# Kernel tuning notes

Measured on AMD Instinct MI355X. Metric: run time of the kernel, lower is better.

The kernel has to match this reference:

```python
import jax, jax.numpy as jnp
import numpy as np

N = 100000   # nodes
D = 8        # in_dim/2 (per-node phase dim)
H = 256      # hidden_dim
E = 1600000  # directed edges (avg degree 16)


def setup_inputs() -> dict:
    key = jax.random.key(0)
    ks = jax.random.split(key, 8)
    q = jax.random.normal(ks[0], (N, D), jnp.float32)
    p = jax.random.normal(ks[1], (N, D), jnp.float32)
    # per-node diagonal positive-definite mass matrix (what get_mass() produces:
    # diag(relu(diag(.)) + 1e-4)); keep it well-conditioned for the inverse.
    m_diag = jax.random.uniform(ks[2], (N, D), jnp.float32) + 0.5
    M = jax.vmap(jnp.diag)(m_diag)  # [N, D, D]
    src = jax.random.randint(ks[3], (E,), 0, N, dtype=jnp.int32)
    off = jax.random.randint(ks[4], (E,), 1, N, dtype=jnp.int32)
    dst = ((src + off) % N).astype(jnp.int32)  # guaranteed no self-edges (euclid>0)
    W1 = jax.random.normal(ks[5], (D, H), jnp.float32) / jnp.sqrt(D)
    b1 = jnp.zeros((H,), jnp.float32)
    W2 = jax.random.normal(ks[6], (H, D), jnp.float32) / jnp.sqrt(H)
    b2 = jnp.zeros((D,), jnp.float32)
    gravity = jnp.ones((1, 1), jnp.float32)
    return {"q": q, "p": p, "M": M, "src": src, "dst": dst,
            "W1": W1, "b1": b1, "W2": W2, "b2": b2, "gravity": gravity}


def _gcn(x, src, dst, norm_src, norm_dst, W, b, n_nodes):
    # DGL GraphConv norm='both': D_out^{-1/2} on src, sum-aggregate, D_in^{-1/2} on dst
    m = (x * norm_src[:, None])[src]                       # [E, F]
    agg = jax.ops.segment_sum(m, dst, num_segments=n_nodes)
    return (agg * norm_dst[:, None]) @ W + b


def reference(q, p, M, src, dst, W1, b1, W2, b2, gravity):
    n = q.shape[0]
    ones_e = jnp.ones(src.shape[0], q.dtype)
    out_deg = jax.ops.segment_sum(ones_e, src, num_segments=n)
    in_deg = jax.ops.segment_sum(ones_e, dst, num_segments=n)
    norm_src = jnp.where(out_deg > 0, out_deg, 1.0) ** -0.5
    norm_dst = jnp.where(in_deg > 0, in_deg, 1.0) ** -0.5

    def P_scalar(qq):
        # ConvGNN: GraphConv -> ReLU -> GraphConv, residual add
        h = jax.nn.relu(_gcn(qq, src, dst, norm_src, norm_dst, W1, b1, n))
        h = _gcn(h, src, dst, norm_src, norm_dst, W2, b2, n) + qq      # [N, D]
        euclid = jnp.linalg.norm(h[src] - h[dst], axis=-1)             # [E]
        masses = M[src] * M[dst]                                       # [E, D, D]
        return 0.5 * jnp.sum(gravity[0, 0] * masses / euclid[:, None, None])

    # dHdq = grad of potential P w.r.t q (torch.autograd.grad in original)
    dHdQ = jax.grad(P_scalar)(q)
    # dHdp: per-node p_i @ inv(M_i)  (self-loop graph, degree 1 per node)
    dHdP = jnp.linalg.solve(jnp.swapaxes(M, -1, -2), p[..., None])[..., 0]
    return jnp.concatenate([dHdQ, dHdP], axis=-1)  # [N, 2D]
```

## Files before the change

### kernel.cpp

```cpp
#include <hip/hip_runtime.h>
#include <hip/hip_fp16.h>

#define DD 8
#define HH 256
#define CH 8192
#define PAYBITS 17
#define PAYMASK 0x1FFFF
#define WPITCH 20


__global__ void k_coarse(const int* __restrict__ src, const int* __restrict__ dst,
                         int* __restrict__ gHistIn, int* __restrict__ gHistOut,
                         int NB, int E) {
    __shared__ int hIn[256], hOut[256];
    if (threadIdx.x < 256) { hIn[threadIdx.x] = 0; hOut[threadIdx.x] = 0; }
    __syncthreads();
    int lo = blockIdx.x * CH;
    int hi = min(lo + CH, E);
    for (int i = lo + threadIdx.x; i < hi; i += blockDim.x) {
        atomicAdd(&hIn[dst[i] >> 9], 1);
        atomicAdd(&hOut[src[i] >> 9], 1);
    }
    __syncthreads();
    if (threadIdx.x < NB) {
        int ci = hIn[threadIdx.x], co = hOut[threadIdx.x];
        if (ci) atomicAdd(&gHistIn[threadIdx.x], ci);
        if (co) atomicAdd(&gHistOut[threadIdx.x], co);
    }
}

__global__ void k_cscan(const int* __restrict__ gHistIn, const int* __restrict__ gHistOut,
                        int* __restrict__ cStartIn, int* __restrict__ cStartOut,
                        int* __restrict__ cCurIn, int* __restrict__ cCurOut,
                        int NB, int E) {
    __shared__ int s[256];
#pragma unroll
    for (int dir = 0; dir < 2; dir++) {
        const int* gh = dir ? gHistOut : gHistIn;
        int* cs = dir ? cStartOut : cStartIn;
        int* cc = dir ? cCurOut : cCurIn;
        int v = (threadIdx.x < NB) ? gh[threadIdx.x] : 0;
        s[threadIdx.x] = v;
        __syncthreads();
        for (int off = 1; off < 256; off <<= 1) {
            int t = (threadIdx.x >= off) ? s[threadIdx.x - off] : 0;
            __syncthreads();
            s[threadIdx.x] += t;
            __syncthreads();
        }
        if (threadIdx.x < NB) {
            int ex = s[threadIdx.x] - v;
            cs[threadIdx.x] = ex;
            cc[threadIdx.x] = ex;
        }
        if (threadIdx.x == 0) cs[NB] = E;
        __syncthreads();
    }
}

__global__ void k_part2(const int* __restrict__ src, const int* __restrict__ dst,
                        int* __restrict__ cCurIn, int* __restrict__ cCurOut,
                        int* __restrict__ P_in, int* __restrict__ P_out,
                        int NB, int E) {
    int dir = blockIdx.y;
    const int* key = dir ? src : dst;
    const int* pay = dir ? dst : src;
    int* cCur = dir ? cCurOut : cCurIn;
    int* P    = dir ? P_out   : P_in;
    __shared__ int h[256];
    if (threadIdx.x < 256) h[threadIdx.x] = 0;
    __syncthreads();
    int lo = blockIdx.x * CH;
    int hi = min(lo + CH, E);
    for (int i = lo + threadIdx.x; i < hi; i += blockDim.x)
        atomicAdd(&h[key[i] >> 9], 1);
    __syncthreads();
    if (threadIdx.x < NB) {
        int c = h[threadIdx.x];
        h[threadIdx.x] = c ? atomicAdd(&cCur[threadIdx.x], c) : 0;
    }
    __syncthreads();
    for (int i = lo + threadIdx.x; i < hi; i += blockDim.x) {
        int k = key[i];
        int pos = atomicAdd(&h[k >> 9], 1);
        P[pos] = ((k & 511) << PAYBITS) | pay[i];
    }
}

__launch_bounds__(512)
__global__ void k_fine2(const int* __restrict__ cStartIn, const int* __restrict__ cStartOut,
                        const int* __restrict__ P_in, const int* __restrict__ P_out,
                        int* __restrict__ start_in, int* __restrict__ start_out,
                        int* __restrict__ csr_in, int* __restrict__ csr_out, int N) {
    int dir = blockIdx.y;
    const int* cStart = dir ? cStartOut : cStartIn;
    const int* P      = dir ? P_out     : P_in;
    int* start        = dir ? start_out : start_in;
    int* csr          = dir ? csr_out   : csr_in;
    __shared__ int cnt[512], scn[512];
    int b = blockIdx.x;
    int lo = cStart[b], hi = cStart[b + 1];
    cnt[threadIdx.x] = 0;
    __syncthreads();
    for (int i = lo + threadIdx.x; i < hi; i += 512)
        atomicAdd(&cnt[P[i] >> PAYBITS], 1);
    __syncthreads();
    int own = cnt[threadIdx.x];
    scn[threadIdx.x] = own;
    __syncthreads();
    for (int off = 1; off < 512; off <<= 1) {
        int t = (threadIdx.x >= off) ? scn[threadIdx.x - off] : 0;
        __syncthreads();
        scn[threadIdx.x] += t;
        __syncthreads();
    }
    int base = lo + scn[threadIdx.x] - own;
    int node = (b << 9) + threadIdx.x;
    if (node < N) start[node] = base;
    cnt[threadIdx.x] = base;
    __syncthreads();
    for (int i = lo + threadIdx.x; i < hi; i += 512) {
        int p = P[i];
        int pos = atomicAdd(&cnt[p >> PAYBITS], 1);
        csr[pos] = p & PAYMASK;
    }
}

__global__ void k_prep(const float* __restrict__ q, const float* __restrict__ p,
                       const float* __restrict__ M,
                       const float* __restrict__ W1, const float* __restrict__ W2,
                       float* __restrict__ W12p,
                       int* __restrict__ start_in, int* __restrict__ start_out,
                       float* __restrict__ a, float* __restrict__ b,
                       __half2* __restrict__ hm, float* __restrict__ qn,
                       float* __restrict__ out, int N, int E) {
    int t = blockIdx.x * blockDim.x + threadIdx.x;
    if (t == 0) { start_in[N] = E; start_out[N] = E; }
    if (t < HH * DD) {
        int j = t >> 3, dd = t & 7;
        W12p[j * WPITCH + dd]     = W1[dd * HH + j];
        W12p[j * WPITCH + 8 + dd] = W2[j * DD + dd];
    }
    int v = t;
    if (v >= N) return;
    int ei1 = (v + 1 < N) ? start_in[v + 1]  : E;
    int eo1 = (v + 1 < N) ? start_out[v + 1] : E;
    float din  = (float)(ei1 - start_in[v]);
    float dout = (float)(eo1 - start_out[v]);
    float av = 1.0f / sqrtf(dout > 0.f ? dout : 1.f);
    float bv = 1.0f / sqrtf(din  > 0.f ? din  : 1.f);
    a[v] = av; b[v] = bv;
#pragma unroll
    for (int d = 0; d < DD; d++) {
        float m = M[(size_t)v * DD * DD + d * (DD + 1)];
        __half2 hmv;
        hmv.x = __float2half(0.f);
        hmv.y = __float2half(m);
        hm[(size_t)v * DD + d] = hmv;
        qn[(size_t)v * DD + d] = av * q[(size_t)v * DD + d];
        out[(size_t)v * 2 * DD + DD + d] = p[(size_t)v * DD + d] / m;
    }
}

static __device__ __forceinline__
void acc_h8(uint4 r, float acc[8]) {
    float2 f;
    f = __half22float2(*(__half2*)&r.x); acc[0] += f.x; acc[1] += f.y;
    f = __half22float2(*(__half2*)&r.y); acc[2] += f.x; acc[3] += f.y;
    f = __half22float2(*(__half2*)&r.z); acc[4] += f.x; acc[5] += f.y;
    f = __half22float2(*(__half2*)&r.w); acc[6] += f.x; acc[7] += f.y;
}

static __device__ __forceinline__
void unpack_hm(uint4 r0, uint4 r1, float h[8], float m[8]) {
    float2 f;
    f = __half22float2(*(__half2*)&r0.x); h[0] = f.x; m[0] = f.y;
    f = __half22float2(*(__half2*)&r0.y); h[1] = f.x; m[1] = f.y;
    f = __half22float2(*(__half2*)&r0.z); h[2] = f.x; m[2] = f.y;
    f = __half22float2(*(__half2*)&r0.w); h[3] = f.x; m[3] = f.y;
    f = __half22float2(*(__half2*)&r1.x); h[4] = f.x; m[4] = f.y;
    f = __half22float2(*(__half2*)&r1.y); h[5] = f.x; m[5] = f.y;
    f = __half22float2(*(__half2*)&r1.z); h[6] = f.x; m[6] = f.y;
    f = __half22float2(*(__half2*)&r1.w); h[7] = f.x; m[7] = f.y;
}

static __device__ __forceinline__
void gather_h8(const int* __restrict__ csr, const __half* __restrict__ x,
               int e, int e1, float acc[8]) {
    for (; e + 3 < e1; e += 4) {
        int u0 = csr[e], u1 = csr[e + 1], u2 = csr[e + 2], u3 = csr[e + 3];
        uint4 r0 = *(const uint4*)(x + (size_t)u0 * DD);
        uint4 r1 = *(const uint4*)(x + (size_t)u1 * DD);
        uint4 r2 = *(const uint4*)(x + (size_t)u2 * DD);
        uint4 r3 = *(const uint4*)(x + (size_t)u3 * DD);
        acc_h8(r0, acc); acc_h8(r1, acc); acc_h8(r2, acc); acc_h8(r3, acc);
    }
    for (; e < e1; e++) {
        uint4 r = *(const uint4*)(x + (size_t)csr[e] * DD);
        acc_h8(r, acc);
    }
}


__launch_bounds__(256)
__global__ void k_agg_node(const int* __restrict__ start, const int* __restrict__ csr,
                           const float* __restrict__ x, float* __restrict__ y, int N) {
    int t = blockIdx.x * 256 + threadIdx.x;
    int v = t >> 1, half = t & 1;
    if (v >= N) return;
    int e0 = start[v], e1 = start[v + 1];
    int mid = e0 + ((e1 - e0) >> 1);
    int e = half ? mid : e0, hi = half ? e1 : mid;
    float acc[8] = {0.f, 0.f, 0.f, 0.f, 0.f, 0.f, 0.f, 0.f};
    for (; e + 1 < hi; e += 2) {
        int u0 = csr[e], u1 = csr[e + 1];
        const float4* p0 = (const float4*)(x + (size_t)u0 * DD);
        const float4* p1 = (const float4*)(x + (size_t)u1 * DD);
        float4 a0 = p0[0], b0 = p0[1], a1 = p1[0], b1 = p1[1];
        acc[0] += a0.x + a1.x; acc[1] += a0.y + a1.y;
        acc[2] += a0.z + a1.z; acc[3] += a0.w + a1.w;
        acc[4] += b0.x + b1.x; acc[5] += b0.y + b1.y;
        acc[6] += b0.z + b1.z; acc[7] += b0.w + b1.w;
    }
    if (e < hi) {
        const float4* p = (const float4*)(x + (size_t)csr[e] * DD);
        float4 a0 = p[0], b0 = p[1];
        acc[0] += a0.x; acc[1] += a0.y; acc[2] += a0.z; acc[3] += a0.w;
        acc[4] += b0.x; acc[5] += b0.y; acc[6] += b0.z; acc[7] += b0.w;
    }
#pragma unroll
    for (int k = 0; k < 8; k++) acc[k] += __shfl_xor(acc[k], 1);
    if (!half) {
        float4* yp = (float4*)(y + (size_t)v * DD);
        yp[0] = make_float4(acc[0], acc[1], acc[2], acc[3]);
        yp[1] = make_float4(acc[4], acc[5], acc[6], acc[7]);
    }
}

__launch_bounds__(256)
__global__ void k_h_node(const int* __restrict__ start, const int* __restrict__ csr,
                         const __half* __restrict__ ya, const float* __restrict__ b,
                         const float* __restrict__ q, const float* __restrict__ b2,
                         __half2* __restrict__ hm, int N) {
    int t = blockIdx.x * 256 + threadIdx.x;
    int v = t >> 1, half = t & 1;
    if (v >= N) return;
    int e0 = start[v], e1 = start[v + 1];
    int mid = e0 + ((e1 - e0) >> 1);
    float acc[8] = {0.f, 0.f, 0.f, 0.f, 0.f, 0.f, 0.f, 0.f};
    gather_h8(csr, ya, half ? mid : e0, half ? e1 : mid, acc);
#pragma unroll
    for (int k = 0; k < 8; k++) acc[k] += __shfl_xor(acc[k], 1);
    if (!half) {
        float bv = b[v];
        const float4* qp = (const float4*)(q + (size_t)v * DD);
        float4 q0 = qp[0], q1 = qp[1];
        float hq[8] = {q0.x, q0.y, q0.z, q0.w, q1.x, q1.y, q1.z, q1.w};
        __half2* hp = hm + (size_t)v * DD;
#pragma unroll
        for (int k = 0; k < DD; k++) {
            float hval = fmaf(bv, acc[k], b2[k] + hq[k]);
            __half2 cur = hp[k];
            cur.x = __float2half(hval);
            hp[k] = cur;
        }
    }
}

__launch_bounds__(256)
__global__ void k_gh4(const int* __restrict__ start_in, const int* __restrict__ csr_in,
                      const int* __restrict__ start_out, const int* __restrict__ csr_out,
                      const __half2* __restrict__ hm,
                      const float* __restrict__ b, const float* __restrict__ grav,
                      float* __restrict__ gh, __half* __restrict__ bgh, int N) {
    int t = blockIdx.x * 256 + threadIdx.x;
    int v = t >> 2, sub = t & 3, dir = sub >> 1, half = sub & 1;
    if (v >= N) return;
    const uint4* srec = (const uint4*)(hm + (size_t)v * DD);
    uint4 s0 = srec[0], s1 = srec[1];
    float hv[8], mv[8];
    unpack_hm(s0, s1, hv, mv);
    const int* start = dir ? start_out : start_in;
    const int* csr   = dir ? csr_out   : csr_in;
    int e0 = start[v], e1 = start[v + 1];
    int mid = e0 + ((e1 - e0) >> 1);
    int e = half ? mid : e0, hi = half ? e1 : mid;
    float coef = -0.5f * grav[0];
    float acc[8] = {0.f, 0.f, 0.f, 0.f, 0.f, 0.f, 0.f, 0.f};
    for (; e + 1 < hi; e += 2) {
        int u0 = csr[e], u1 = csr[e + 1];
        const uint4* r0p = (const uint4*)(hm + (size_t)u0 * DD);
        const uint4* r1p = (const uint4*)(hm + (size_t)u1 * DD);
        uint4 x0 = r0p[0], x1 = r0p[1], y0 = r1p[0], y1 = r1p[1];
        float hu0[8], mu0[8], hu1[8], mu1[8];
        unpack_hm(x0, x1, hu0, mu0);
        unpack_hm(y0, y1, hu1, mu1);
        float d0[8], d1[8];
        float e20 = 0.f, S0 = 0.f, e21 = 0.f, S1 = 0.f;
#pragma unroll
        for (int k = 0; k < 8; k++) {
            d0[k] = hv[k] - hu0[k];
            d1[k] = hv[k] - hu1[k];
            e20 = fmaf(d0[k], d0[k], e20);
            e21 = fmaf(d1[k], d1[k], e21);
            S0 = fmaf(mv[k], mu0[k], S0);
            S1 = fmaf(mv[k], mu1[k], S1);
        }
        float r0 = rsqrtf(e20), r1 = rsqrtf(e21);
        float c0 = coef * S0 * r0 * r0 * r0;
        float c1 = coef * S1 * r1 * r1 * r1;
#pragma unroll
        for (int k = 0; k < 8; k++)
            acc[k] = fmaf(c0, d0[k], fmaf(c1, d1[k], acc[k]));
    }
    if (e < hi) {
        int u = csr[e];
        const uint4* rp = (const uint4*)(hm + (size_t)u * DD);
        uint4 x0 = rp[0], x1 = rp[1];
        float hu[8], mu[8];
        unpack_hm(x0, x1, hu, mu);
        float df[8];
        float e2 = 0.f, S = 0.f;
#pragma unroll
        for (int k = 0; k < 8; k++) {
            df[k] = hv[k] - hu[k];
            e2 = fmaf(df[k], df[k], e2);
            S = fmaf(mv[k], mu[k], S);
        }
        float r = rsqrtf(e2);
        float c = coef * S * r * r * r;
#pragma unroll
        for (int k = 0; k < 8; k++) acc[k] = fmaf(c, df[k], acc[k]);
    }
#pragma unroll
    for (int k = 0; k < 8; k++) acc[k] += __shfl_xor(acc[k], 1);
#pragma unroll
    for (int k = 0; k < 8; k++) acc[k] += __shfl_xor(acc[k], 2);
    if (sub == 0) {
        float4* gp = (float4*)(gh + (size_t)v * DD);
        gp[0] = make_float4(acc[0], acc[1], acc[2], acc[3]);
        gp[1] = make_float4(acc[4], acc[5], acc[6], acc[7]);
        float bv = b[v];
        __half2* bp = (__half2*)(bgh + (size_t)v * DD);
        bp[0] = __floats2half2_rn(bv * acc[0], bv * acc[1]);
        bp[1] = __floats2half2_rn(bv * acc[2], bv * acc[3]);
        bp[2] = __floats2half2_rn(bv * acc[4], bv * acc[5]);
        bp[3] = __floats2half2_rn(bv * acc[6], bv * acc[7]);
    }
}

__launch_bounds__(256)
__global__ void k_bgh_node(const int* __restrict__ start, const int* __restrict__ csr,
                           const __half* __restrict__ bgh, float* __restrict__ gq2, int N) {
    int t = blockIdx.x * 256 + threadIdx.x;
    int v = t >> 1, half = t & 1;
    if (v >= N) return;
    int e0 = start[v], e1 = start[v + 1];
    int mid = e0 + ((e1 - e0) >> 1);
    float acc[8] = {0.f, 0.f, 0.f, 0.f, 0.f, 0.f, 0.f, 0.f};
    gather_h8(csr, bgh, half ? mid : e0, half ? e1 : mid, acc);
#pragma unroll
    for (int k = 0; k < 8; k++) acc[k] += __shfl_xor(acc[k], 1);
    if (!half) {
        float4* yp = (float4*)(gq2 + (size_t)v * DD);
        yp[0] = make_float4(acc[0], acc[1], acc[2], acc[3]);
        yp[1] = make_float4(acc[4], acc[5], acc[6], acc[7]);
    }
}

__launch_bounds__(256)
__global__ void k_out_node(const int* __restrict__ start, const int* __restrict__ csr,
                           const __half* __restrict__ gz1b, const float* __restrict__ gh,
                           const float* __restrict__ a, float* __restrict__ out, int N) {
    int t = blockIdx.x * 256 + threadIdx.x;
    int v = t >> 1, half = t & 1;
    if (v >= N) return;
    int e0 = start[v], e1 = start[v + 1];
    int mid = e0 + ((e1 - e0) >> 1);
    float acc[8] = {0.f, 0.f, 0.f, 0.f, 0.f, 0.f, 0.f, 0.f};
    gather_h8(csr, gz1b, half ? mid : e0, half ? e1 : mid, acc);
#pragma unroll
    for (int k = 0; k < 8; k++) acc[k] += __shfl_xor(acc[k], 1);
    if (!half) {
        float av = a[v];
        const float4* gp = (const float4*)(gh + (size_t)v * DD);
        float4 g0 = gp[0], g1 = gp[1];
        float4* op = (float4*)(out + (size_t)v * 2 * DD);
        op[0] = make_float4(fmaf(av, acc[0], g0.x), fmaf(av, acc[1], g0.y),
                            fmaf(av, acc[2], g0.z), fmaf(av, acc[3], g0.w));
        op[1] = make_float4(fmaf(av, acc[4], g1.x), fmaf(av, acc[5], g1.y),
                            fmaf(av, acc[6], g1.z), fmaf(av, acc[7], g1.w));
    }
}


__launch_bounds__(256)
__global__ void k_mlp_fwd(const float* __restrict__ agg1, const float* __restrict__ a,
                          const float* __restrict__ b,
                          const float* __restrict__ W12p, const float* __restrict__ b1,
                          __half* __restrict__ ya, int N) {
    __shared__ float sW[HH * WPITCH];
    __shared__ float sb1[HH];
    for (int i = threadIdx.x; i < HH * WPITCH; i += 256) sW[i] = W12p[i];
    for (int i = threadIdx.x; i < HH; i += 256) sb1[i] = b1[i];
    __syncthreads();
    int t = blockIdx.x * 256 + threadIdx.x;
    int v = t >> 4, l16 = t & 15, sub = (t >> 3) & 1, d = t & 7;
    if (v >= N) return;
    float zl = b[v] * agg1[(size_t)v * DD + d];
    float z[DD];
#pragma unroll
    for (int k = 0; k < DD; k++) z[k] = __shfl(zl, k, 16);
    float acc[DD] = {0.f, 0.f, 0.f, 0.f, 0.f, 0.f, 0.f, 0.f};
    for (int c = 0; c < HH / 16; c += 2) {
        int j0 = (c << 4) | l16, j1 = j0 + 16;
        const float4* w0 = (const float4*)(sW + j0 * WPITCH);
        const float4* w1 = (const float4*)(sW + j1 * WPITCH);
        float4 wa0 = w0[0], wb0 = w0[1], va0 = w0[2], vb0 = w0[3];
        float4 wa1 = w1[0], wb1 = w1[1], va1 = w1[2], vb1 = w1[3];
        float ua0 = fmaf(z[1], wa0.y, fmaf(z[0], wa0.x, sb1[j0]));
        ua0 = fmaf(z[3], wa0.w, fmaf(z[2], wa0.z, ua0));
        float ub0 = fmaf(z[5], wb0.y, z[4] * wb0.x);
        ub0 = fmaf(z[7], wb0.w, fmaf(z[6], wb0.z, ub0));
        float ua1 = fmaf(z[1], wa1.y, fmaf(z[0], wa1.x, sb1[j1]));
        ua1 = fmaf(z[3], wa1.w, fmaf(z[2], wa1.z, ua1));
        float ub1 = fmaf(z[5], wb1.y, z[4] * wb1.x);
        ub1 = fmaf(z[7], wb1.w, fmaf(z[6], wb1.z, ub1));
        float h0 = fmaxf(ua0 + ub0, 0.f);
        float h1 = fmaxf(ua1 + ub1, 0.f);
        acc[0] = fmaf(h0, va0.x, acc[0]); acc[1] = fmaf(h0, va0.y, acc[1]);
        acc[2] = fmaf(h0, va0.z, acc[2]); acc[3] = fmaf(h0, va0.w, acc[3]);
        acc[4] = fmaf(h0, vb0.x, acc[4]); acc[5] = fmaf(h0, vb0.y, acc[5]);
        acc[6] = fmaf(h0, vb0.z, acc[6]); acc[7] = fmaf(h0, vb0.w, acc[7]);
        acc[0] = fmaf(h1, va1.x, acc[0]); acc[1] = fmaf(h1, va1.y, acc[1]);
        acc[2] = fmaf(h1, va1.z, acc[2]); acc[3] = fmaf(h1, va1.w, acc[3]);
        acc[4] = fmaf(h1, vb1.x, acc[4]); acc[5] = fmaf(h1, vb1.y, acc[5]);
        acc[6] = fmaf(h1, vb1.z, acc[6]); acc[7] = fmaf(h1, vb1.w, acc[7]);
    }
#pragma unroll
    for (int m = 1; m < 16; m <<= 1)
#pragma unroll
        for (int k = 0; k < DD; k++) acc[k] += __shfl_xor(acc[k], m);
    float yl = acc[0];
#pragma unroll
    for (int k = 1; k < DD; k++) yl = (d == k) ? acc[k] : yl;
    if (!sub) ya[(size_t)v * DD + d] = __float2half(a[v] * yl);
}

__launch_bounds__(256)
__global__ void k_mlp_bwd(const float* __restrict__ gq2, const float* __restrict__ agg1,
                          const float* __restrict__ a, const float* __restrict__ b,
                          const float* __restrict__ W12p, const float* __restrict__ b1,
                          __half* __restrict__ gz1b, int N) {
    __shared__ float sW[HH * WPITCH];
    __shared__ float sb1[HH];
    for (int i = threadIdx.x; i < HH * WPITCH; i += 256) sW[i] = W12p[i];
    for (int i = threadIdx.x; i < HH; i += 256) sb1[i] = b1[i];
    __syncthreads();
    int t = blockIdx.x * 256 + threadIdx.x;
    int v = t >> 4, l16 = t & 15, sub = (t >> 3) & 1, d = t & 7;
    if (v >= N) return;
    float bv = b[v], av = a[v];
    float zl = bv * agg1[(size_t)v * DD + d];
    float gl = gq2[(size_t)v * DD + d];
    float z[DD], gq[DD];
#pragma unroll
    for (int k = 0; k < DD; k++) { z[k] = __shfl(zl, k, 16); gq[k] = __shfl(gl, k, 16); }
    float gz[DD] = {0.f, 0.f, 0.f, 0.f, 0.f, 0.f, 0.f, 0.f};
    for (int c = 0; c < HH / 16; c += 2) {
        int j0 = (c << 4) | l16, j1 = j0 + 16;
        const float4* w0 = (const float4*)(sW + j0 * WPITCH);
        const float4* w1 = (const float4*)(sW + j1 * WPITCH);
        float4 wa0 = w0[0], wb0 = w0[1], va0 = w0[2], vb0 = w0[3];
        float4 wa1 = w1[0], wb1 = w1[1], va1 = w1[2], vb1 = w1[3];
        float ua0 = fmaf(z[1], wa0.y, fmaf(z[0], wa0.x, sb1[j0]));
        ua0 = fmaf(z[3], wa0.w, fmaf(z[2], wa0.z, ua0));
        float ub0 = fmaf(z[5], wb0.y, z[4] * wb0.x);
        ub0 = fmaf(z[7], wb0.w, fmaf(z[6], wb0.z, ub0));
        float ua1 = fmaf(z[1], wa1.y, fmaf(z[0], wa1.x, sb1[j1]));
        ua1 = fmaf(z[3], wa1.w, fmaf(z[2], wa1.z, ua1));
        float ub1 = fmaf(z[5], wb1.y, z[4] * wb1.x);
        ub1 = fmaf(z[7], wb1.w, fmaf(z[6], wb1.z, ub1));
        float u0 = ua0 + ub0, u1 = ua1 + ub1;
        float ga0 = fmaf(gq[1], va0.y, gq[0] * va0.x);
        ga0 = fmaf(gq[3], va0.w, fmaf(gq[2], va0.z, ga0));
        float gb0 = fmaf(gq[5], vb0.y, gq[4] * vb0.x);
        gb0 = fmaf(gq[7], vb0.w, fmaf(gq[6], vb0.z, gb0));
        float ga1 = fmaf(gq[1], va1.y, gq[0] * va1.x);
        ga1 = fmaf(gq[3], va1.w, fmaf(gq[2], va1.z, ga1));
        float gb1 = fmaf(gq[5], vb1.y, gq[4] * vb1.x);
        gb1 = fmaf(gq[7], vb1.w, fmaf(gq[6], vb1.z, gb1));
        float g0 = (u0 > 0.f) ? av * (ga0 + gb0) : 0.f;
        float g1 = (u1 > 0.f) ? av * (ga1 + gb1) : 0.f;
        gz[0] = fmaf(g0, wa0.x, gz[0]); gz[1] = fmaf(g0, wa0.y, gz[1]);
        gz[2] = fmaf(g0, wa0.z, gz[2]); gz[3] = fmaf(g0, wa0.w, gz[3]);
        gz[4] = fmaf(g0, wb0.x, gz[4]); gz[5] = fmaf(g0, wb0.y, gz[5]);
        gz[6] = fmaf(g0, wb0.z, gz[6]); gz[7] = fmaf(g0, wb0.w, gz[7]);
        gz[0] = fmaf(g1, wa1.x, gz[0]); gz[1] = fmaf(g1, wa1.y, gz[1]);
        gz[2] = fmaf(g1, wa1.z, gz[2]); gz[3] = fmaf(g1, wa1.w, gz[3]);
        gz[4] = fmaf(g1, wb1.x, gz[4]); gz[5] = fmaf(g1, wb1.y, gz[5]);
        gz[6] = fmaf(g1, wb1.z, gz[6]); gz[7] = fmaf(g1, wb1.w, gz[7]);
    }
#pragma unroll
    for (int m = 1; m < 16; m <<= 1)
#pragma unroll
        for (int k = 0; k < DD; k++) gz[k] += __shfl_xor(gz[k], m);
    float out_l = gz[0];
#pragma unroll
    for (int k = 1; k < DD; k++) out_l = (d == k) ? gz[k] : out_l;
    if (!sub) gz1b[(size_t)v * DD + d] = __float2half(bv * out_l);
}


extern "C" void kernel_launch(void* const* d_in, const int* in_sizes, int n_in,
                              void* d_out, int out_size, void* d_ws, size_t ws_size,
                              hipStream_t stream) {
    const float* q    = (const float*)d_in[0];
    const float* p    = (const float*)d_in[1];
    const float* M    = (const float*)d_in[2];
    const int*   src  = (const int*)d_in[3];
    const int*   dst  = (const int*)d_in[4];
    const float* W1   = (const float*)d_in[5];
    const float* b1   = (const float*)d_in[6];
    const float* W2   = (const float*)d_in[7];
    const float* b2   = (const float*)d_in[8];
    const float* grav = (const float*)d_in[9];
    float* out = (float*)d_out;

    int N = in_sizes[0] / DD;
    int E = in_sizes[3];
    size_t n = (size_t)N;
    int NB = (N + 511) >> 9;

    float*   ws   = (float*)d_ws;
    float*   a_   = ws;
    float*   b_   = ws + n;
    float*   qn   = ws + 2  * n;
    float*   agg1 = ws + 10 * n;
    float*   gh   = ws + 18 * n;
    __half2* hm   = (__half2*)(ws + 26 * n);
    __half*  ya   = (__half*)(ws + 34 * n);
    __half*  bgh  = (__half*)(ws + 38 * n);
    __half*  gz1b = (__half*)(ws + 42 * n);
    float*   gq2  = qn;

    int* iw        = (int*)(ws + 46 * n);
    int* csr_in    = iw;
    int* csr_out   = iw + (size_t)E;
    int* start_in  = iw + 2 * (size_t)E;
    int* start_out = start_in + n + 1;
    int* gHistIn   = start_out + n + 1;
    int* gHistOut  = gHistIn + 256;
    int* cStartIn  = gHistOut + 256;
    int* cStartOut = cStartIn + NB + 1;
    int* cCurIn    = cStartOut + NB + 1;
    int* cCurOut   = cCurIn + NB;
    int* iwEnd     = cCurOut + NB;
    float* W12p    = (float*)iwEnd;
    int* intAfter  = (int*)(W12p + HH * WPITCH);
    int* P_in  = (E <= 16 * (long long)n) ? (int*)ws            : intAfter;
    int* P_out = (E <= 16 * (long long)n) ? (int*)(ws + 16 * n) : intAfter + E;

    hipMemsetAsync(gHistIn, 0, 512 * sizeof(int), stream);

    const int tb = 256;
    int gbN  = (N + tb - 1) / tb;
    int gb2  = (2 * N + tb - 1) / tb;
    int gb4  = (4 * N + tb - 1) / tb;
    int gb16 = (int)((16 * n + tb - 1) / tb);
    int gbC  = (E + CH - 1) / CH;

    k_coarse  <<<gbC, tb, 0, stream>>>(src, dst, gHistIn, gHistOut, NB, E);
    k_cscan   <<<1, 256, 0, stream>>>(gHistIn, gHistOut, cStartIn, cStartOut,
                                      cCurIn, cCurOut, NB, E);
    k_part2   <<<dim3(gbC, 2), tb, 0, stream>>>(src, dst, cCurIn, cCurOut,
                                                P_in, P_out, NB, E);
    k_fine2   <<<dim3(NB, 2), 512, 0, stream>>>(cStartIn, cStartOut, P_in, P_out,
                                                start_in, start_out, csr_in, csr_out, N);
    k_prep    <<<gbN, tb, 0, stream>>>(q, p, M, W1, W2, W12p, start_in, start_out,
                                       a_, b_, hm, qn, out, N, E);

    k_agg_node<<<gb2, tb, 0, stream>>>(start_in, csr_in, qn, agg1, N);
    k_mlp_fwd <<<gb16, tb, 0, stream>>>(agg1, a_, b_, W12p, b1, ya, N);
    k_h_node  <<<gb2, tb, 0, stream>>>(start_in, csr_in, ya, b_, q, b2, hm, N);
    k_gh4     <<<gb4, tb, 0, stream>>>(start_in, csr_in, start_out, csr_out,
                                       hm, b_, grav, gh, bgh, N);
    k_bgh_node<<<gb2, tb, 0, stream>>>(start_out, csr_out, bgh, gq2, N);
    k_mlp_bwd <<<gb16, tb, 0, stream>>>(gq2, agg1, a_, b_, W12p, b1, gz1b, N);
    k_out_node<<<gb2, tb, 0, stream>>>(start_out, csr_out, gz1b, gh, a_, out, N);
}
```

Before: 343.0 us.

## Fuse neighbor aggregation into forward and backward MLP kernels

The first-layer CSR aggregation is merged into the forward MLP kernel, and the bgh gather is merged into the backward MLP kernel. In each fused kernel 16 lanes per node stride over the edges and reduce with shuffles. This removes two kernel launches and the round trip of the gq2 intermediate through global memory. In exchange, the gather now runs inside kernels that load the full weight table into shared memory per block, which may lower occupancy and spreads 16 lanes over an average of 16 edges.

```diff
diff --git a/kernel.cpp b/kernel.cpp
--- a/kernel.cpp
+++ b/kernel.cpp
@@ -7,6 +7,7 @@
 #define PAYBITS 17
 #define PAYMASK 0x1FFFF
 #define WPITCH 20
+
 
 
 __global__ void k_coarse(const int* __restrict__ src, const int* __restrict__ dst,
@@ -201,40 +202,75 @@
     }
 }
 
-
 __launch_bounds__(256)
-__global__ void k_agg_node(const int* __restrict__ start, const int* __restrict__ csr,
-                           const float* __restrict__ x, float* __restrict__ y, int N) {
+__global__ void k_agg_mlp_fwd(const int* __restrict__ start, const int* __restrict__ csr,
+                              const float* __restrict__ qn,
+                              const float* __restrict__ a, const float* __restrict__ b,
+                              const float* __restrict__ W12p, const float* __restrict__ b1,
+                              float* __restrict__ agg1, __half* __restrict__ ya, int N) {
+    __shared__ float sW[HH * WPITCH];
+    __shared__ float sb1[HH];
+    for (int i = threadIdx.x; i < HH * WPITCH; i += 256) sW[i] = W12p[i];
+    for (int i = threadIdx.x; i < HH; i += 256) sb1[i] = b1[i];
+    __syncthreads();
     int t = blockIdx.x * 256 + threadIdx.x;
-    int v = t >> 1, half = t & 1;
+    int v = t >> 4, l16 = t & 15, sub = (t >> 3) & 1, d = t & 7;
     if (v >= N) return;
     int e0 = start[v], e1 = start[v + 1];
-    int mid = e0 + ((e1 - e0) >> 1);
-    int e = half ? mid : e0, hi = half ? e1 : mid;
-    float acc[8] = {0.f, 0.f, 0.f, 0.f, 0.f, 0.f, 0.f, 0.f};
-    for (; e + 1 < hi; e += 2) {
-        int u0 = csr[e], u1 = csr[e + 1];
-        const float4* p0 = (const float4*)(x + (size_t)u0 * DD);
-        const float4* p1 = (const float4*)(x + (size_t)u1 * DD);
-        float4 a0 = p0[0], b0 = p0[1], a1 = p1[0], b1 = p1[1];
-        acc[0] += a0.x + a1.x; acc[1] += a0.y + a1.y;
-        acc[2] += a0.z + a1.z; acc[3] += a0.w + a1.w;
-        acc[4] += b0.x + b1.x; acc[5] += b0.y + b1.y;
-        acc[6] += b0.z + b1.z; acc[7] += b0.w + b1.w;
-    }
-    if (e < hi) {
-        const float4* p = (const float4*)(x + (size_t)csr[e] * DD);
-        float4 a0 = p[0], b0 = p[1];
-        acc[0] += a0.x; acc[1] += a0.y; acc[2] += a0.z; acc[3] += a0.w;
-        acc[4] += b0.x; acc[5] += b0.y; acc[6] += b0.z; acc[7] += b0.w;
-    }
-#pragma unroll
-    for (int k = 0; k < 8; k++) acc[k] += __shfl_xor(acc[k], 1);
-    if (!half) {
-        float4* yp = (float4*)(y + (size_t)v * DD);
-        yp[0] = make_float4(acc[0], acc[1], acc[2], acc[3]);
-        yp[1] = make_float4(acc[4], acc[5], acc[6], acc[7]);
-    }
+    float ag[DD] = {0.f, 0.f, 0.f, 0.f, 0.f, 0.f, 0.f, 0.f};
+    for (int e = e0 + l16; e < e1; e += 16) {
+        const float4* p0 = (const float4*)(qn + (size_t)csr[e] * DD);
+        float4 a0 = p0[0], b0 = p0[1];
+        ag[0] += a0.x; ag[1] += a0.y; ag[2] += a0.z; ag[3] += a0.w;
+        ag[4] += b0.x; ag[5] += b0.y; ag[6] += b0.z; ag[7] += b0.w;
+    }
+#pragma unroll
+    for (int m = 1; m < 16; m <<= 1)
+#pragma unroll
+        for (int k = 0; k < DD; k++) ag[k] += __shfl_xor(ag[k], m);
+    if (l16 < 2) {
+        float4 val = l16 ? make_float4(ag[4], ag[5], ag[6], ag[7])
+                         : make_float4(ag[0], ag[1], ag[2], ag[3]);
+        ((float4*)(agg1 + (size_t)v * DD))[l16] = val;
+    }
+    float bv = b[v];
+    float z[DD];
+#pragma unroll
+    for (int k = 0; k < DD; k++) z[k] = bv * ag[k];
+    float acc[DD] = {0.f, 0.f, 0.f, 0.f, 0.f, 0.f, 0.f, 0.f};
+    for (int c = 0; c < HH / 16; c += 2) {
+        int j0 = (c << 4) | l16, j1 = j0 + 16;
+        const float4* w0 = (const float4*)(sW + j0 * WPITCH);
+        const float4* w1 = (const float4*)(sW + j1 * WPITCH);
+        float4 wa0 = w0[0], wb0 = w0[1], va0 = w0[2], vb0 = w0[3];
+        float4 wa1 = w1[0], wb1 = w1[1], va1 = w1[2], vb1 = w1[3];
+        float ua0 = fmaf(z[1], wa0.y, fmaf(z[0], wa0.x, sb1[j0]));
+        ua0 = fmaf(z[3], wa0.w, fmaf(z[2], wa0.z, ua0));
+        float ub0 = fmaf(z[5], wb0.y, z[4] * wb0.x);
+        ub0 = fmaf(z[7], wb0.w, fmaf(z[6], wb0.z, ub0));
+        float ua1 = fmaf(z[1], wa1.y, fmaf(z[0], wa1.x, sb1[j1]));
+        ua1 = fmaf(z[3], wa1.w, fmaf(z[2], wa1.z, ua1));
+        float ub1 = fmaf(z[5], wb1.y, z[4] * wb1.x);
+        ub1 = fmaf(z[7], wb1.w, fmaf(z[6], wb1.z, ub1));
+        float h0 = fmaxf(ua0 + ub0, 0.f);
+        float h1 = fmaxf(ua1 + ub1, 0.f);
+        acc[0] = fmaf(h0, va0.x, acc[0]); acc[1] = fmaf(h0, va0.y, acc[1]);
+        acc[2] = fmaf(h0, va0.z, acc[2]); acc[3] = fmaf(h0, va0.w, acc[3]);
+        acc[4] = fmaf(h0, vb0.x, acc[4]); acc[5] = fmaf(h0, vb0.y, acc[5]);
+        acc[6] = fmaf(h0, vb0.z, acc[6]); acc[7] = fmaf(h0, vb0.w, acc[7]);
+        acc[0] = fmaf(h1, va1.x, acc[0]); acc[1] = fmaf(h1, va1.y, acc[1]);
+        acc[2] = fmaf(h1, va1.z, acc[2]); acc[3] = fmaf(h1, va1.w, acc[3]);
+        acc[4] = fmaf(h1, vb1.x, acc[4]); acc[5] = fmaf(h1, vb1.y, acc[5]);
+        acc[6] = fmaf(h1, vb1.z, acc[6]); acc[7] = fmaf(h1, vb1.w, acc[7]);
+    }
+#pragma unroll
+    for (int m = 1; m < 16; m <<= 1)
+#pragma unroll
+        for (int k = 0; k < DD; k++) acc[k] += __shfl_xor(acc[k], m);
+    float yl = acc[0];
+#pragma unroll
+    for (int k = 1; k < DD; k++) yl = (d == k) ? acc[k] : yl;
+    if (!sub) ya[(size_t)v * DD + d] = __float2half(a[v] * yl);
 }
 
 __launch_bounds__(256)
@@ -350,55 +386,12 @@
 }
 
 __launch_bounds__(256)
-__global__ void k_bgh_node(const int* __restrict__ start, const int* __restrict__ csr,
-                           const __half* __restrict__ bgh, float* __restrict__ gq2, int N) {
-    int t = blockIdx.x * 256 + threadIdx.x;
-    int v = t >> 1, half = t & 1;
-    if (v >= N) return;
-    int e0 = start[v], e1 = start[v + 1];
-    int mid = e0 + ((e1 - e0) >> 1);
-    float acc[8] = {0.f, 0.f, 0.f, 0.f, 0.f, 0.f, 0.f, 0.f};
-    gather_h8(csr, bgh, half ? mid : e0, half ? e1 : mid, acc);
-#pragma unroll
-    for (int k = 0; k < 8; k++) acc[k] += __shfl_xor(acc[k], 1);
-    if (!half) {
-        float4* yp = (float4*)(gq2 + (size_t)v * DD);
-        yp[0] = make_float4(acc[0], acc[1], acc[2], acc[3]);
-        yp[1] = make_float4(acc[4], acc[5], acc[6], acc[7]);
-    }
-}
-
-__launch_bounds__(256)
-__global__ void k_out_node(const int* __restrict__ start, const int* __restrict__ csr,
-                           const __half* __restrict__ gz1b, const float* __restrict__ gh,
-                           const float* __restrict__ a, float* __restrict__ out, int N) {
-    int t = blockIdx.x * 256 + threadIdx.x;
-    int v = t >> 1, half = t & 1;
-    if (v >= N) return;
-    int e0 = start[v], e1 = start[v + 1];
-    int mid = e0 + ((e1 - e0) >> 1);
-    float acc[8] = {0.f, 0.f, 0.f, 0.f, 0.f, 0.f, 0.f, 0.f};
-    gather_h8(csr, gz1b, half ? mid : e0, half ? e1 : mid, acc);
-#pragma unroll
-    for (int k = 0; k < 8; k++) acc[k] += __shfl_xor(acc[k], 1);
-    if (!half) {
-        float av = a[v];
-        const float4* gp = (const float4*)(gh + (size_t)v * DD);
-        float4 g0 = gp[0], g1 = gp[1];
-        float4* op = (float4*)(out + (size_t)v * 2 * DD);
-        op[0] = make_float4(fmaf(av, acc[0], g0.x), fmaf(av, acc[1], g0.y),
-                            fmaf(av, acc[2], g0.z), fmaf(av, acc[3], g0.w));
-        op[1] = make_float4(fmaf(av, acc[4], g1.x), fmaf(av, acc[5], g1.y),
-                            fmaf(av, acc[6], g1.z), fmaf(av, acc[7], g1.w));
-    }
-}
-
-
-__launch_bounds__(256)
-__global__ void k_mlp_fwd(const float* __restrict__ agg1, const float* __restrict__ a,
-                          const float* __restrict__ b,
-                          const float* __restrict__ W12p, const float* __restrict__ b1,
-                          __half* __restrict__ ya, int N) {
+__global__ void k_bgh_mlp_bwd(const int* __restrict__ start, const int* __restrict__ csr,
+                              const __half* __restrict__ bgh,
+                              const float* __restrict__ agg1,
+                              const float* __restrict__ a, const float* __restrict__ b,
+                              const float* __restrict__ W12p, const float* __restrict__ b1,
+                              __half* __restrict__ gz1b, int N) {
     __shared__ float sW[HH * WPITCH];
     __shared__ float sb1[HH];
     for (int i = threadIdx.x; i < HH * WPITCH; i += 256) sW[i] = W12p[i];
@@ -407,65 +400,21 @@
     int t = blockIdx.x * 256 + threadIdx.x;
     int v = t >> 4, l16 = t & 15, sub = (t >> 3) & 1, d = t & 7;
     if (v >= N) return;
-    float zl = b[v] * agg1[(size_t)v * DD + d];
-    float z[DD];
-#pragma unroll
-    for (int k = 0; k < DD; k++) z[k] = __shfl(zl, k, 16);
-    float acc[DD] = {0.f, 0.f, 0.f, 0.f, 0.f, 0.f, 0.f, 0.f};
-    for (int c = 0; c < HH / 16; c += 2) {
-        int j0 = (c << 4) | l16, j1 = j0 + 16;
-        const float4* w0 = (const float4*)(sW + j0 * WPITCH);
-        const float4* w1 = (const float4*)(sW + j1 * WPITCH);
-        float4 wa0 = w0[0], wb0 = w0[1], va0 = w0[2], vb0 = w0[3];
-        float4 wa1 = w1[0], wb1 = w1[1], va1 = w1[2], vb1 = w1[3];
-        float ua0 = fmaf(z[1], wa0.y, fmaf(z[0], wa0.x, sb1[j0]));
-        ua0 = fmaf(z[3], wa0.w, fmaf(z[2], wa0.z, ua0));
-        float ub0 = fmaf(z[5], wb0.y, z[4] * wb0.x);
-        ub0 = fmaf(z[7], wb0.w, fmaf(z[6], wb0.z, ub0));
-        float ua1 = fmaf(z[1], wa1.y, fmaf(z[0], wa1.x, sb1[j1]));
-        ua1 = fmaf(z[3], wa1.w, fmaf(z[2], wa1.z, ua1));
-        float ub1 = fmaf(z[5], wb1.y, z[4] * wb1.x);
-        ub1 = fmaf(z[7], wb1.w, fmaf(z[6], wb1.z, ub1));
-        float h0 = fmaxf(ua0 + ub0, 0.f);
-        float h1 = fmaxf(ua1 + ub1, 0.f);
-        acc[0] = fmaf(h0, va0.x, acc[0]); acc[1] = fmaf(h0, va0.y, acc[1]);
-        acc[2] = fmaf(h0, va0.z, acc[2]); acc[3] = fmaf(h0, va0.w, acc[3]);
-        acc[4] = fmaf(h0, vb0.x, acc[4]); acc[5] = fmaf(h0, vb0.y, acc[5]);
-        acc[6] = fmaf(h0, vb0.z, acc[6]); acc[7] = fmaf(h0, vb0.w, acc[7]);
-        acc[0] = fmaf(h1, va1.x, acc[0]); acc[1] = fmaf(h1, va1.y, acc[1]);
-        acc[2] = fmaf(h1, va1.z, acc[2]); acc[3] = fmaf(h1, va1.w, acc[3]);
-        acc[4] = fmaf(h1, vb1.x, acc[4]); acc[5] = fmaf(h1, vb1.y, acc[5]);
-        acc[6] = fmaf(h1, vb1.z, acc[6]); acc[7] = fmaf(h1, vb1.w, acc[7]);
+    int e0 = start[v], e1 = start[v + 1];
+    float gq[DD] = {0.f, 0.f, 0.f, 0.f, 0.f, 0.f, 0.f, 0.f};
+    for (int e = e0 + l16; e < e1; e += 16) {
+        uint4 r = *(const uint4*)(bgh + (size_t)csr[e] * DD);
+        acc_h8(r, gq);
     }
 #pragma unroll
     for (int m = 1; m < 16; m <<= 1)
 #pragma unroll
-        for (int k = 0; k < DD; k++) acc[k] += __shfl_xor(acc[k], m);
-    float yl = acc[0];
-#pragma unroll
-    for (int k = 1; k < DD; k++) yl = (d == k) ? acc[k] : yl;
-    if (!sub) ya[(size_t)v * DD + d] = __float2half(a[v] * yl);
-}
-
-__launch_bounds__(256)
-__global__ void k_mlp_bwd(const float* __restrict__ gq2, const float* __restrict__ agg1,
-                          const float* __restrict__ a, const float* __restrict__ b,
-                          const float* __restrict__ W12p, const float* __restrict__ b1,
-                          __half* __restrict__ gz1b, int N) {
-    __shared__ float sW[HH * WPITCH];
-    __shared__ float sb1[HH];
-    for (int i = threadIdx.x; i < HH * WPITCH; i += 256) sW[i] = W12p[i];
-    for (int i = threadIdx.x; i < HH; i += 256) sb1[i] = b1[i];
-    __syncthreads();
-    int t = blockIdx.x * 256 + threadIdx.x;
-    int v = t >> 4, l16 = t & 15, sub = (t >> 3) & 1, d = t & 7;
-    if (v >= N) return;
+        for (int k = 0; k < DD; k++) gq[k] += __shfl_xor(gq[k], m);
     float bv = b[v], av = a[v];
     float zl = bv * agg1[(size_t)v * DD + d];
-    float gl = gq2[(size_t)v * DD + d];
-    float z[DD], gq[DD];
-#pragma unroll
-    for (int k = 0; k < DD; k++) { z[k] = __shfl(zl, k, 16); gq[k] = __shfl(gl, k, 16); }
+    float z[DD];
+#pragma unroll
+    for (int k = 0; k < DD; k++) z[k] = __shfl(zl, k, 16);
     float gz[DD] = {0.f, 0.f, 0.f, 0.f, 0.f, 0.f, 0.f, 0.f};
     for (int c = 0; c < HH / 16; c += 2) {
         int j0 = (c << 4) | l16, j1 = j0 + 16;
@@ -511,6 +460,31 @@
     if (!sub) gz1b[(size_t)v * DD + d] = __float2half(bv * out_l);
 }
 
+__launch_bounds__(256)
+__global__ void k_out_node(const int* __restrict__ start, const int* __restrict__ csr,
+                           const __half* __restrict__ gz1b, const float* __restrict__ gh,
+                           const float* __restrict__ a, float* __restrict__ out, int N) {
+    int t = blockIdx.x * 256 + threadIdx.x;
+    int v = t >> 1, half = t & 1;
+    if (v >= N) return;
+    int e0 = start[v], e1 = start[v + 1];
+    int mid = e0 + ((e1 - e0) >> 1);
+    float acc[8] = {0.f, 0.f, 0.f, 0.f, 0.f, 0.f, 0.f, 0.f};
+    gather_h8(csr, gz1b, half ? mid : e0, half ? e1 : mid, acc);
+#pragma unroll
+    for (int k = 0; k < 8; k++) acc[k] += __shfl_xor(acc[k], 1);
+    if (!half) {
+        float av = a[v];
+        const float4* gp = (const float4*)(gh + (size_t)v * DD);
+        float4 g0 = gp[0], g1 = gp[1];
+        float4* op = (float4*)(out + (size_t)v * 2 * DD);
+        op[0] = make_float4(fmaf(av, acc[0], g0.x), fmaf(av, acc[1], g0.y),
+                            fmaf(av, acc[2], g0.z), fmaf(av, acc[3], g0.w));
+        op[1] = make_float4(fmaf(av, acc[4], g1.x), fmaf(av, acc[5], g1.y),
+                            fmaf(av, acc[6], g1.z), fmaf(av, acc[7], g1.w));
+    }
+}
+
 
 extern "C" void kernel_launch(void* const* d_in, const int* in_sizes, int n_in,
                               void* d_out, int out_size, void* d_ws, size_t ws_size,
@@ -542,7 +516,6 @@
     __half*  ya   = (__half*)(ws + 34 * n);
     __half*  bgh  = (__half*)(ws + 38 * n);
     __half*  gz1b = (__half*)(ws + 42 * n);
-    float*   gq2  = qn;
 
     int* iw        = (int*)(ws + 46 * n);
     int* csr_in    = iw;
@@ -580,12 +553,12 @@
     k_prep    <<<gbN, tb, 0, stream>>>(q, p, M, W1, W2, W12p, start_in, start_out,
                                        a_, b_, hm, qn, out, N, E);
 
-    k_agg_node<<<gb2, tb, 0, stream>>>(start_in, csr_in, qn, agg1, N);
-    k_mlp_fwd <<<gb16, tb, 0, stream>>>(agg1, a_, b_, W12p, b1, ya, N);
+    k_agg_mlp_fwd<<<gb16, tb, 0, stream>>>(start_in, csr_in, qn, a_, b_,
+                                           W12p, b1, agg1, ya, N);
     k_h_node  <<<gb2, tb, 0, stream>>>(start_in, csr_in, ya, b_, q, b2, hm, N);
     k_gh4     <<<gb4, tb, 0, stream>>>(start_in, csr_in, start_out, csr_out,
                                        hm, b_, grav, gh, bgh, N);
-    k_bgh_node<<<gb2, tb, 0, stream>>>(start_out, csr_out, bgh, gq2, N);
-    k_mlp_bwd <<<gb16, tb, 0, stream>>>(gq2, agg1, a_, b_, W12p, b1, gz1b, N);
+    k_bgh_mlp_bwd<<<gb16, tb, 0, stream>>>(start_out, csr_out, bgh, agg1, a_, b_,
+                                           W12p, b1, gz1b, N);
     k_out_node<<<gb2, tb, 0, stream>>>(start_out, csr_out, gz1b, gh, a_, out, N);
 }
```

Result: faster. 332.3 us (-3.1%).
